# Performance work log

Hardware: AMD Instinct MI355X
Metric: run time of the kernel (lower is better)

Reference implementation:

```python
import jax, jax.numpy as jnp
import numpy as np

B, S, D, H = 4, 2048, 1024, 16
HD = D // H

def setup_inputs() -> dict:
    key = jax.random.key(0)
    ks = jax.random.split(key, 5)
    s = 1.0 / np.sqrt(D)
    return {
        "x": jax.random.normal(ks[0], (B, S, D), dtype=jnp.float32),
        "Wq": jax.random.normal(ks[1], (D, D), dtype=jnp.float32) * s,
        "Wk": jax.random.normal(ks[2], (D, D), dtype=jnp.float32) * s,
        "Wv": jax.random.normal(ks[3], (D, D), dtype=jnp.float32) * s,
        "Wo": jax.random.normal(ks[4], (D, D), dtype=jnp.float32) * s,
        "bo": jnp.zeros((D,), dtype=jnp.float32),
    }

def reference(x, Wq, Wk, Wv, Wo, bo):
    b, n, _ = x.shape
    # torch Linear: x @ W.T ; split heads -> [b, h, n, hd]
    def proj(W):
        return (x @ W.T).reshape(b, n, H, HD).transpose(0, 2, 1, 3)
    q, k, v = proj(Wq), proj(Wk), proj(Wv)
    scores = jnp.einsum('bhqd,bhkd->bhqk', q, k)  # [b,h,n,n]
    causal = jnp.triu(jnp.ones((n, n), dtype=bool), k=1)
    scores = jnp.where(causal, -jnp.inf, scores)
    attn = jax.nn.softmax(scores / np.sqrt(HD), axis=-1)  # dropout p=0.0 (eval)
    ctx = jnp.einsum('bhqk,bhkd->bhqd', attn, v)
    ctx = ctx.transpose(0, 2, 1, 3).reshape(b, n, D)
    return ctx @ Wo.T + bo
```

## Files before the change

### kernel.cpp

```cpp
#include <hip/hip_runtime.h>
#include <stdint.h>
#include <cmath>

#define BATCH 4
#define SEQ   2048
#define DM    1024
#define NH    16
#define HDIM  64
#define MROWS (BATCH*SEQ)

typedef __attribute__((ext_vector_type(8)))  __bf16 bf16x8;
typedef __attribute__((ext_vector_type(8)))  unsigned short u16x8;
typedef __attribute__((ext_vector_type(4)))  float f32x4;
typedef __attribute__((ext_vector_type(16))) float f32x16;
typedef __attribute__((ext_vector_type(4)))  unsigned int u32x4;

__device__ __forceinline__ unsigned short f2bf(float f) {
  unsigned u = __float_as_uint(f);
  u = (u + 0x7FFFu + ((u >> 16) & 1u)) >> 16;
  return (unsigned short)u;
}

__device__ __forceinline__ f32x4 mfma_bf16(bf16x8 a, bf16x8 b, f32x4 c) {
  return __builtin_amdgcn_mfma_f32_16x16x32_bf16(a, b, c, 0, 0, 0);
}
__device__ __forceinline__ f32x16 mfma32(bf16x8 a, bf16x8 b, f32x16 c) {
  return __builtin_amdgcn_mfma_f32_32x32x16_bf16(a, b, c, 0, 0, 0);
}

__device__ __forceinline__ unsigned cvtpk(float lo, float hi) {
  unsigned r;
  asm("v_cvt_pk_bf16_f32 %0, %1, %2" : "=v"(r) : "v"(lo), "v"(hi));
  return r;
}
__device__ __forceinline__ void permswap(unsigned &a, unsigned &b) {
  asm volatile("v_permlane32_swap_b32 %0, %1" : "+v"(a), "+v"(b));
}
__device__ __forceinline__ f32x16 zero16() {
  f32x16 z;
#pragma unroll
  for (int i = 0; i < 16; ++i) z[i] = 0.f;
  return z;
}

typedef const __attribute__((address_space(1))) unsigned int* as1_u32p;
typedef __attribute__((address_space(3))) unsigned int* as3_u32p;

__device__ __forceinline__ void gload16(const void* g, void* l) {
  __builtin_amdgcn_global_load_lds((as1_u32p)g, (as3_u32p)l, 16, 0, 0);
}

__global__ void cvt_f32_bf16(const float* __restrict__ src,
                             unsigned short* __restrict__ dst, int n4) {
  int i = blockIdx.x * blockDim.x + threadIdx.x;
  int stride = gridDim.x * blockDim.x;
  for (; i < n4; i += stride) {
    float4 v = ((const float4*)src)[i];
    ushort4 o;
    o.x = f2bf(v.x); o.y = f2bf(v.y); o.z = f2bf(v.z); o.w = f2bf(v.w);
    ((ushort4*)dst)[i] = o;
  }
}

__device__ __forceinline__ void gemm_tile_mainloop(
    const unsigned short* __restrict__ A, const unsigned short* __restrict__ Bw,
    int rowBase, int colBase,
    unsigned short* As, unsigned short* Bs,
    f32x4 acc[4][4], int tid)
{
  const int wid = tid >> 6, lane = tid & 63;
  const int wm = wid >> 1, wn = wid & 1;
  const unsigned short* Atile = A + (size_t)rowBase * DM;
  const unsigned short* Btile = Bw + (size_t)colBase * DM;

  for (int k0 = 0; k0 < DM; k0 += 64) {
#pragma unroll
    for (int j = 0; j < 4; ++j) {
      int c = j * 256 + tid;
      int row = c >> 3;
      int inB = (c & 7) * 16;
      int srcE = row * DM + k0 + ((inB ^ ((row & 7) << 4)) >> 1);
      gload16(Atile + srcE, As + (size_t)(j * 256 + wid * 64) * 8);
    }
#pragma unroll
    for (int j = 0; j < 4; ++j) {
      int c = j * 256 + tid;
      int row = c >> 3;
      int inB = (c & 7) * 16;
      int srcE = row * DM + k0 + ((inB ^ ((row & 7) << 4)) >> 1);
      gload16(Btile + srcE, Bs + (size_t)(j * 256 + wid * 64) * 8);
    }
    __syncthreads();

#pragma unroll
    for (int s2 = 0; s2 < 2; ++s2) {
      bf16x8 af[4], bfv[4];
#pragma unroll
      for (int m = 0; m < 4; ++m) {
        int row = wm * 64 + m * 16 + (lane & 15);
        int off = row * 128 + ((s2 * 64 + ((lane >> 4) * 16)) ^ ((row & 7) << 4));
        af[m] = *(const bf16x8*)((const char*)As + off);
      }
#pragma unroll
      for (int n = 0; n < 4; ++n) {
        int row = wn * 64 + n * 16 + (lane & 15);
        int off = row * 128 + ((s2 * 64 + ((lane >> 4) * 16)) ^ ((row & 7) << 4));
        bfv[n] = *(const bf16x8*)((const char*)Bs + off);
      }
#pragma unroll
      for (int m = 0; m < 4; ++m)
#pragma unroll
        for (int n = 0; n < 4; ++n)
          acc[m][n] = mfma_bf16(af[m], bfv[n], acc[m][n]);
    }
    __syncthreads();
  }
}

__global__ __launch_bounds__(256, 2) void gemm_qkv(
    const unsigned short* __restrict__ xb,
    const unsigned short* __restrict__ Wqb, const unsigned short* __restrict__ Wkb,
    const unsigned short* __restrict__ Wvb,
    unsigned short* __restrict__ Qd, unsigned short* __restrict__ Kd,
    unsigned short* __restrict__ Vd)
{
  __shared__ unsigned short As[128 * 64];
  __shared__ unsigned short Bs[128 * 64];
  const int tid = threadIdx.x;
  const int z = blockIdx.z;
  const unsigned short* W = (z == 0) ? Wqb : (z == 1) ? Wkb : Wvb;
  unsigned short* dst = (z == 0) ? Qd : (z == 1) ? Kd : Vd;
  const int rowBase = blockIdx.x * 128, colBase = blockIdx.y * 128;

  f32x4 acc[4][4];
#pragma unroll
  for (int m = 0; m < 4; ++m)
#pragma unroll
    for (int n = 0; n < 4; ++n) acc[m][n] = (f32x4){0.f, 0.f, 0.f, 0.f};

  gemm_tile_mainloop(xb, W, rowBase, colBase, As, Bs, acc, tid);

  const int wid = tid >> 6, lane = tid & 63;
  const int wm = wid >> 1, wn = wid & 1;
#pragma unroll
  for (int m = 0; m < 4; ++m)
#pragma unroll
    for (int n = 0; n < 4; ++n)
#pragma unroll
      for (int r = 0; r < 4; ++r) {
        int grow = rowBase + wm * 64 + m * 16 + ((lane >> 4) * 4) + r;
        int gcol = colBase + wn * 64 + n * 16 + (lane & 15);
        int b = grow >> 11, s = grow & (SEQ - 1);
        int h = gcol >> 6, hd = gcol & 63;
        dst[(((size_t)(b * NH + h)) * SEQ + s) * HDIM + hd] = f2bf(acc[m][n][r]);
      }
}

__global__ __launch_bounds__(256, 2) void gemm_out(
    const unsigned short* __restrict__ ctx, const unsigned short* __restrict__ Wob,
    const float* __restrict__ bo, float* __restrict__ out)
{
  __shared__ unsigned short As[128 * 64];
  __shared__ unsigned short Bs[128 * 64];
  const int tid = threadIdx.x;
  const int rowBase = blockIdx.x * 128, colBase = blockIdx.y * 128;

  f32x4 acc[4][4];
#pragma unroll
  for (int m = 0; m < 4; ++m)
#pragma unroll
    for (int n = 0; n < 4; ++n) acc[m][n] = (f32x4){0.f, 0.f, 0.f, 0.f};

  gemm_tile_mainloop(ctx, Wob, rowBase, colBase, As, Bs, acc, tid);

  const int wid = tid >> 6, lane = tid & 63;
  const int wm = wid >> 1, wn = wid & 1;
#pragma unroll
  for (int m = 0; m < 4; ++m)
#pragma unroll
    for (int n = 0; n < 4; ++n)
#pragma unroll
      for (int r = 0; r < 4; ++r) {
        int grow = rowBase + wm * 64 + m * 16 + ((lane >> 4) * 4) + r;
        int gcol = colBase + wn * 64 + n * 16 + (lane & 15);
        out[(size_t)grow * DM + gcol] = acc[m][n][r] + bo[gcol];
      }
}

__global__ void transpose_v(const unsigned short* __restrict__ Vd,
                            unsigned short* __restrict__ VT)
{
  __shared__ unsigned short tile[64 * 72];
  const int tid = threadIdx.x;
  const int bh = blockIdx.y, s0 = blockIdx.x * 64;
  const unsigned short* src = Vd + (size_t)bh * SEQ * HDIM + (size_t)s0 * HDIM;
#pragma unroll
  for (int j = 0; j < 2; ++j) {
    int c = j * 256 + tid;
    int r = c >> 3, c0 = (c & 7) * 8;
    *(u16x8*)(tile + r * 72 + c0) = *(const u16x8*)(src + r * HDIM + c0);
  }
  __syncthreads();
  unsigned short* dst = VT + (size_t)bh * HDIM * SEQ + s0;
#pragma unroll
  for (int j = 0; j < 2; ++j) {
    int c = j * 256 + tid;
    int d = c >> 3, c0 = (c & 7) * 8;
    u16x8 v;
#pragma unroll
    for (int e = 0; e < 8; ++e) v[e] = tile[(c0 + e) * 72 + d];
    *(u16x8*)(dst + (size_t)d * SEQ + c0) = v;
  }
}

__global__ __launch_bounds__(256, 2) void attn_fwd2(
    const unsigned short* __restrict__ Qg, const unsigned short* __restrict__ Kg,
    const unsigned short* __restrict__ VTg, unsigned short* __restrict__ ctx)
{
  __shared__ unsigned short smem[16384];

  const int tid = threadIdx.x, wid = tid >> 6, lane = tid & 63;
  const int hi = lane >> 5, lq = lane & 31;
  const int qb = (int)gridDim.x - 1 - (int)blockIdx.x;
  const int bh = blockIdx.y;
  const unsigned short* Qp = Qg  + (size_t)bh * SEQ * HDIM;
  const unsigned short* Kp = Kg  + (size_t)bh * SEQ * HDIM;
  const unsigned short* Vp = VTg + (size_t)bh * HDIM * SEQ;
  const int qw0 = qb * 128 + wid * 32;

  bf16x8 qf[4];
  {
    const unsigned short* qrow = Qp + (size_t)(qw0 + lq) * HDIM + hi * 8;
#pragma unroll
    for (int ks = 0; ks < 4; ++ks) qf[ks] = *(const bf16x8*)(qrow + ks * 16);
  }

  f32x16 o0 = zero16(), o1 = zero16();
  float m_run = -INFINITY, l_run = 0.f;

  const int nt = 2 * qb + 2;

  auto stageK = [&](int t, int buf) {
#pragma unroll
    for (int j = 0; j < 2; ++j) {
      int c = j * 256 + tid;
      int row = c >> 3, inB = (c & 7) * 16;
      gload16(Kp + (size_t)(t * 64 + row) * HDIM + ((inB ^ ((row & 7) << 4)) >> 1),
              smem + buf * 4096 + (size_t)(j * 256 + wid * 64) * 8);
    }
  };
  auto stageV = [&](int t, int buf) {
#pragma unroll
    for (int j = 0; j < 2; ++j) {
      int c = j * 256 + tid;
      int row = c >> 3, inB = (c & 7) * 16;
      gload16(Vp + (size_t)row * SEQ + t * 64 + ((inB ^ ((row & 7) << 4)) >> 1),
              smem + 8192 + buf * 4096 + (size_t)(j * 256 + wid * 64) * 8);
    }
  };

  stageK(0, 0); stageV(0, 0);
  __syncthreads();

  for (int t = 0; t < nt; ++t) {
    const int cur = t & 1;
    if (t + 1 < nt) { stageK(t + 1, cur ^ 1); stageV(t + 1, cur ^ 1); }

    if (t * 64 <= qw0 + 31) {
      const unsigned short* Kl = smem + cur * 4096;
      f32x16 s0 = zero16(), s1 = zero16();
#pragma unroll
      for (int ks = 0; ks < 4; ++ks) {
        int r0 = lq, r1 = lq + 32;
        int col = (ks * 32 + hi * 16);
        bf16x8 a0 = *(const bf16x8*)((const char*)Kl + r0 * 128 + (col ^ ((r0 & 7) << 4)));
        bf16x8 a1 = *(const bf16x8*)((const char*)Kl + r1 * 128 + (col ^ ((r1 & 7) << 4)));
        s0 = mfma32(a0, qf[ks], s0);
        s1 = mfma32(a1, qf[ks], s1);
      }

      if (t * 64 + 63 > qw0) {
        const int q = qw0 + lq;
        const int kb = t * 64 + 4 * hi;
#pragma unroll
        for (int r = 0; r < 16; ++r) {
          int k0 = kb + (r & 3) + 8 * (r >> 2);
          if (k0 > q)      s0[r] = -INFINITY;
          if (k0 + 32 > q) s1[r] = -INFINITY;
        }
      }

      float pmax = s0[0];
#pragma unroll
      for (int r = 1; r < 16; ++r) pmax = fmaxf(pmax, s0[r]);
#pragma unroll
      for (int r = 0; r < 16; ++r) pmax = fmaxf(pmax, s1[r]);
      pmax = fmaxf(pmax, __shfl_xor(pmax, 32, 64));

      if (!__all(pmax - m_run <= 64.0f)) {
        float mn = fmaxf(m_run, pmax);
        float alpha = __expf((m_run - mn) * 0.125f);
        l_run *= alpha;
#pragma unroll
        for (int r = 0; r < 16; ++r) { o0[r] *= alpha; o1[r] *= alpha; }
        m_run = mn;
      }

      float rsum = 0.f;
#pragma unroll
      for (int r = 0; r < 16; ++r) {
        s0[r] = __expf((s0[r] - m_run) * 0.125f); rsum += s0[r];
      }
#pragma unroll
      for (int r = 0; r < 16; ++r) {
        s1[r] = __expf((s1[r] - m_run) * 0.125f); rsum += s1[r];
      }
      rsum += __shfl_xor(rsum, 32, 64);
      l_run += rsum;

      bf16x8 pfr[4];
#pragma unroll
      for (int h2 = 0; h2 < 2; ++h2) {
        {
          unsigned va = cvtpk(s0[h2 * 8 + 0], s0[h2 * 8 + 1]);
          unsigned vb = cvtpk(s0[h2 * 8 + 4], s0[h2 * 8 + 5]);
          unsigned vc = cvtpk(s0[h2 * 8 + 2], s0[h2 * 8 + 3]);
          unsigned vd = cvtpk(s0[h2 * 8 + 6], s0[h2 * 8 + 7]);
          permswap(va, vb); permswap(vc, vd);
          u32x4 tt; tt.x = va; tt.y = vc; tt.z = vb; tt.w = vd;
          pfr[h2] = __builtin_bit_cast(bf16x8, tt);
        }
        {
          unsigned va = cvtpk(s1[h2 * 8 + 0], s1[h2 * 8 + 1]);
          unsigned vb = cvtpk(s1[h2 * 8 + 4], s1[h2 * 8 + 5]);
          unsigned vc = cvtpk(s1[h2 * 8 + 2], s1[h2 * 8 + 3]);
          unsigned vd = cvtpk(s1[h2 * 8 + 6], s1[h2 * 8 + 7]);
          permswap(va, vb); permswap(vc, vd);
          u32x4 tt; tt.x = va; tt.y = vc; tt.z = vb; tt.w = vd;
          pfr[2 + h2] = __builtin_bit_cast(bf16x8, tt);
        }
      }

      const unsigned short* Vl = smem + 8192 + cur * 4096;
#pragma unroll
      for (int ks = 0; ks < 4; ++ks) {
        int r0 = lq, r1 = lq + 32;
        int col = (ks * 32 + hi * 16);
        bf16x8 va0 = *(const bf16x8*)((const char*)Vl + r0 * 128 + (col ^ ((r0 & 7) << 4)));
        bf16x8 va1 = *(const bf16x8*)((const char*)Vl + r1 * 128 + (col ^ ((r1 & 7) << 4)));
        o0 = mfma32(va0, pfr[ks], o0);
        o1 = mfma32(va1, pfr[ks], o1);
      }
    }
    __syncthreads();
  }

  const float invl = 1.0f / l_run;
  unsigned short* Ot = smem;
  const int q = wid * 32 + lq;
#pragma unroll
  for (int r2 = 0; r2 < 16; r2 += 2) {
    int d = (r2 & 3) + 8 * (r2 >> 2) + 4 * hi;
    unsigned w0 = cvtpk(o0[r2] * invl, o0[r2 + 1] * invl);
    *(unsigned*)((char*)Ot + q * 128 + ((2 * d) ^ ((q & 7) << 4))) = w0;
    int d2 = d + 32;
    unsigned w1 = cvtpk(o1[r2] * invl, o1[r2 + 1] * invl);
    *(unsigned*)((char*)Ot + q * 128 + ((2 * d2) ^ ((q & 7) << 4))) = w1;
  }
  __syncthreads();

  const int b = bh >> 4, h = bh & 15;
#pragma unroll
  for (int i = 0; i < 4; ++i) {
    int idx = i * 256 + tid;
    int qq = idx >> 3, c16 = (idx & 7) * 8;
    bf16x8 v = *(const bf16x8*)((const char*)Ot + qq * 128 + ((2 * c16) ^ ((qq & 7) << 4)));
    *(bf16x8*)(ctx + ((size_t)(b * SEQ) + qb * 128 + qq) * DM + h * 64 + c16) = v;
  }
}

extern "C" void kernel_launch(void* const* d_in, const int* in_sizes, int n_in,
                              void* d_out, int out_size, void* d_ws, size_t ws_size,
                              hipStream_t stream)
{
  (void)in_sizes; (void)n_in; (void)out_size; (void)ws_size;
  const float* x  = (const float*)d_in[0];
  const float* Wq = (const float*)d_in[1];
  const float* Wk = (const float*)d_in[2];
  const float* Wv = (const float*)d_in[3];
  const float* Wo = (const float*)d_in[4];
  const float* bo = (const float*)d_in[5];
  float* out = (float*)d_out;

  char* ws = (char*)d_ws;
  unsigned short* xb  = (unsigned short*)(ws);
  unsigned short* Wqb = (unsigned short*)(ws + (size_t)16 * 1048576);
  unsigned short* Wkb = (unsigned short*)(ws + (size_t)18 * 1048576);
  unsigned short* Wvb = (unsigned short*)(ws + (size_t)20 * 1048576);
  unsigned short* Wob = (unsigned short*)(ws + (size_t)22 * 1048576);
  unsigned short* Qd  = (unsigned short*)(ws + (size_t)24 * 1048576);
  unsigned short* Kd  = (unsigned short*)(ws + (size_t)40 * 1048576);
  unsigned short* Vd  = (unsigned short*)(ws + (size_t)56 * 1048576);
  unsigned short* ctxb= (unsigned short*)(ws + (size_t)72 * 1048576);
  unsigned short* VT  = xb;

  cvt_f32_bf16<<<2048, 256, 0, stream>>>(x,  xb,  MROWS * DM / 4);
  cvt_f32_bf16<<<256,  256, 0, stream>>>(Wq, Wqb, DM * DM / 4);
  cvt_f32_bf16<<<256,  256, 0, stream>>>(Wk, Wkb, DM * DM / 4);
  cvt_f32_bf16<<<256,  256, 0, stream>>>(Wv, Wvb, DM * DM / 4);
  cvt_f32_bf16<<<256,  256, 0, stream>>>(Wo, Wob, DM * DM / 4);

  gemm_qkv<<<dim3(MROWS / 128, DM / 128, 3), 256, 0, stream>>>(xb, Wqb, Wkb, Wvb, Qd, Kd, Vd);
  transpose_v<<<dim3(SEQ / 64, BATCH * NH), 256, 0, stream>>>(Vd, VT);
  attn_fwd2<<<dim3(SEQ / 128, BATCH * NH), 256, 0, stream>>>(Qd, Kd, VT, ctxb);
  gemm_out<<<dim3(MROWS / 128, DM / 128, 1), 256, 0, stream>>>(ctxb, Wob, bo, out);
}
```

Baseline: 291.7 us.

## Pair causal query blocks per CTA, triple-buffer K/V, merge weight conversions

Each attention block now processes two query tiles, qb and NQB-1-qb, so the causal work per CTA is balanced and the grid is halved. K/V staging moves from double to triple buffering, prefetching two tiles ahead with explicit vmcnt waits and raw barriers in place of __syncthreads. MFMA sections are bracketed with s_setprio. The four weight conversion launches are merged into one kernel. The costs are more LDS per block, fewer CTAs (512) for the GPU to spread across its CUs, and the added complexity of hand-written waitcnt accounting.

```diff
diff --git a/kernel.cpp b/kernel.cpp
--- a/kernel.cpp
+++ b/kernel.cpp
@@ -8,6 +8,7 @@
 #define NH    16
 #define HDIM  64
 #define MROWS (BATCH*SEQ)
+#define NQB   16
 
 typedef __attribute__((ext_vector_type(8)))  __bf16 bf16x8;
 typedef __attribute__((ext_vector_type(8)))  unsigned short u16x8;
@@ -62,6 +63,23 @@
   }
 }
 
+__global__ void cvt_w4(const float* __restrict__ s0, const float* __restrict__ s1,
+                       const float* __restrict__ s2, const float* __restrict__ s3,
+                       unsigned short* __restrict__ d0, unsigned short* __restrict__ d1,
+                       unsigned short* __restrict__ d2, unsigned short* __restrict__ d3,
+                       int n4) {
+  const float* src = (blockIdx.y == 0) ? s0 : (blockIdx.y == 1) ? s1 : (blockIdx.y == 2) ? s2 : s3;
+  unsigned short* dst = (blockIdx.y == 0) ? d0 : (blockIdx.y == 1) ? d1 : (blockIdx.y == 2) ? d2 : d3;
+  int i = blockIdx.x * blockDim.x + threadIdx.x;
+  int stride = gridDim.x * blockDim.x;
+  for (; i < n4; i += stride) {
+    float4 v = ((const float4*)src)[i];
+    ushort4 o;
+    o.x = f2bf(v.x); o.y = f2bf(v.y); o.z = f2bf(v.z); o.w = f2bf(v.w);
+    ((ushort4*)dst)[i] = o;
+  }
+}
+
 __device__ __forceinline__ void gemm_tile_mainloop(
     const unsigned short* __restrict__ A, const unsigned short* __restrict__ Bw,
     int rowBase, int colBase,
@@ -213,32 +231,19 @@
   }
 }
 
-__global__ __launch_bounds__(256, 2) void attn_fwd2(
+__global__ __launch_bounds__(256, 2) void attn_fwd3(
     const unsigned short* __restrict__ Qg, const unsigned short* __restrict__ Kg,
     const unsigned short* __restrict__ VTg, unsigned short* __restrict__ ctx)
 {
-  __shared__ unsigned short smem[16384];
+  __shared__ unsigned short smem[24576];
 
   const int tid = threadIdx.x, wid = tid >> 6, lane = tid & 63;
   const int hi = lane >> 5, lq = lane & 31;
-  const int qb = (int)gridDim.x - 1 - (int)blockIdx.x;
   const int bh = blockIdx.y;
   const unsigned short* Qp = Qg  + (size_t)bh * SEQ * HDIM;
   const unsigned short* Kp = Kg  + (size_t)bh * SEQ * HDIM;
   const unsigned short* Vp = VTg + (size_t)bh * HDIM * SEQ;
-  const int qw0 = qb * 128 + wid * 32;
-
-  bf16x8 qf[4];
-  {
-    const unsigned short* qrow = Qp + (size_t)(qw0 + lq) * HDIM + hi * 8;
-#pragma unroll
-    for (int ks = 0; ks < 4; ++ks) qf[ks] = *(const bf16x8*)(qrow + ks * 16);
-  }
-
-  f32x16 o0 = zero16(), o1 = zero16();
-  float m_run = -INFINITY, l_run = 0.f;
-
-  const int nt = 2 * qb + 2;
+  const int b = bh >> 4, h = bh & 15;
 
   auto stageK = [&](int t, int buf) {
 #pragma unroll
@@ -255,127 +260,153 @@
       int c = j * 256 + tid;
       int row = c >> 3, inB = (c & 7) * 16;
       gload16(Vp + (size_t)row * SEQ + t * 64 + ((inB ^ ((row & 7) << 4)) >> 1),
-              smem + 8192 + buf * 4096 + (size_t)(j * 256 + wid * 64) * 8);
+              smem + 12288 + buf * 4096 + (size_t)(j * 256 + wid * 64) * 8);
     }
   };
 
-  stageK(0, 0); stageV(0, 0);
-  __syncthreads();
-
-  for (int t = 0; t < nt; ++t) {
-    const int cur = t & 1;
-    if (t + 1 < nt) { stageK(t + 1, cur ^ 1); stageV(t + 1, cur ^ 1); }
-
-    if (t * 64 <= qw0 + 31) {
-      const unsigned short* Kl = smem + cur * 4096;
-      f32x16 s0 = zero16(), s1 = zero16();
-#pragma unroll
-      for (int ks = 0; ks < 4; ++ks) {
-        int r0 = lq, r1 = lq + 32;
-        int col = (ks * 32 + hi * 16);
-        bf16x8 a0 = *(const bf16x8*)((const char*)Kl + r0 * 128 + (col ^ ((r0 & 7) << 4)));
-        bf16x8 a1 = *(const bf16x8*)((const char*)Kl + r1 * 128 + (col ^ ((r1 & 7) << 4)));
-        s0 = mfma32(a0, qf[ks], s0);
-        s1 = mfma32(a1, qf[ks], s1);
+  for (int half = 0; half < 2; ++half) {
+    const int qb = half == 0 ? (int)blockIdx.x : (NQB - 1 - (int)blockIdx.x);
+    const int qw0 = qb * 128 + wid * 32;
+
+    bf16x8 qf[4];
+    {
+      const unsigned short* qrow = Qp + (size_t)(qw0 + lq) * HDIM + hi * 8;
+#pragma unroll
+      for (int ks = 0; ks < 4; ++ks) qf[ks] = *(const bf16x8*)(qrow + ks * 16);
+    }
+
+    f32x16 o0 = zero16(), o1 = zero16();
+    float m_run = -INFINITY, l_run = 0.f;
+    const int nt = 2 * qb + 2;
+
+    stageK(0, 0); stageV(0, 0);
+    stageK(1, 1); stageV(1, 1);
+    asm volatile("s_waitcnt vmcnt(4)" ::: "memory");
+    __builtin_amdgcn_s_barrier();
+
+    for (int t = 0; t < nt; ++t) {
+      const int cur = t % 3;
+      const bool pf = (t + 2) < nt;
+      if (pf) { int nb = (t + 2) % 3; stageK(t + 2, nb); stageV(t + 2, nb); }
+
+      if (t * 64 <= qw0 + 31) {
+        const unsigned short* Kl = smem + cur * 4096;
+        f32x16 s0 = zero16(), s1 = zero16();
+        __builtin_amdgcn_s_setprio(1);
+#pragma unroll
+        for (int ks = 0; ks < 4; ++ks) {
+          int r0 = lq, r1 = lq + 32;
+          int col = (ks * 32 + hi * 16);
+          bf16x8 a0 = *(const bf16x8*)((const char*)Kl + r0 * 128 + (col ^ ((r0 & 7) << 4)));
+          bf16x8 a1 = *(const bf16x8*)((const char*)Kl + r1 * 128 + (col ^ ((r1 & 7) << 4)));
+          s0 = mfma32(a0, qf[ks], s0);
+          s1 = mfma32(a1, qf[ks], s1);
+        }
+        __builtin_amdgcn_s_setprio(0);
+
+        if (t * 64 + 63 > qw0) {
+          const int q = qw0 + lq;
+          const int kb = t * 64 + 4 * hi;
+#pragma unroll
+          for (int r = 0; r < 16; ++r) {
+            int k0 = kb + (r & 3) + 8 * (r >> 2);
+            if (k0 > q)      s0[r] = -INFINITY;
+            if (k0 + 32 > q) s1[r] = -INFINITY;
+          }
+        }
+
+        float pmax = s0[0];
+#pragma unroll
+        for (int r = 1; r < 16; ++r) pmax = fmaxf(pmax, s0[r]);
+#pragma unroll
+        for (int r = 0; r < 16; ++r) pmax = fmaxf(pmax, s1[r]);
+        pmax = fmaxf(pmax, __shfl_xor(pmax, 32, 64));
+
+        if (!__all(pmax - m_run <= 64.0f)) {
+          float mn = fmaxf(m_run, pmax);
+          float alpha = __expf((m_run - mn) * 0.125f);
+          l_run *= alpha;
+#pragma unroll
+          for (int r = 0; r < 16; ++r) { o0[r] *= alpha; o1[r] *= alpha; }
+          m_run = mn;
+        }
+
+        float rsum = 0.f;
+#pragma unroll
+        for (int r = 0; r < 16; ++r) {
+          s0[r] = __expf((s0[r] - m_run) * 0.125f); rsum += s0[r];
+        }
+#pragma unroll
+        for (int r = 0; r < 16; ++r) {
+          s1[r] = __expf((s1[r] - m_run) * 0.125f); rsum += s1[r];
+        }
+        rsum += __shfl_xor(rsum, 32, 64);
+        l_run += rsum;
+
+        bf16x8 pfr[4];
+#pragma unroll
+        for (int h2 = 0; h2 < 2; ++h2) {
+          {
+            unsigned va = cvtpk(s0[h2 * 8 + 0], s0[h2 * 8 + 1]);
+            unsigned vb = cvtpk(s0[h2 * 8 + 4], s0[h2 * 8 + 5]);
+            unsigned vc = cvtpk(s0[h2 * 8 + 2], s0[h2 * 8 + 3]);
+            unsigned vd = cvtpk(s0[h2 * 8 + 6], s0[h2 * 8 + 7]);
+            permswap(va, vb); permswap(vc, vd);
+            u32x4 tt; tt.x = va; tt.y = vc; tt.z = vb; tt.w = vd;
+            pfr[h2] = __builtin_bit_cast(bf16x8, tt);
+          }
+          {
+            unsigned va = cvtpk(s1[h2 * 8 + 0], s1[h2 * 8 + 1]);
+            unsigned vb = cvtpk(s1[h2 * 8 + 4], s1[h2 * 8 + 5]);
+            unsigned vc = cvtpk(s1[h2 * 8 + 2], s1[h2 * 8 + 3]);
+            unsigned vd = cvtpk(s1[h2 * 8 + 6], s1[h2 * 8 + 7]);
+            permswap(va, vb); permswap(vc, vd);
+            u32x4 tt; tt.x = va; tt.y = vc; tt.z = vb; tt.w = vd;
+            pfr[2 + h2] = __builtin_bit_cast(bf16x8, tt);
+          }
+        }
+
+        const unsigned short* Vl = smem + 12288 + cur * 4096;
+        __builtin_amdgcn_s_setprio(1);
+#pragma unroll
+        for (int ks = 0; ks < 4; ++ks) {
+          int r0 = lq, r1 = lq + 32;
+          int col = (ks * 32 + hi * 16);
+          bf16x8 va0 = *(const bf16x8*)((const char*)Vl + r0 * 128 + (col ^ ((r0 & 7) << 4)));
+          bf16x8 va1 = *(const bf16x8*)((const char*)Vl + r1 * 128 + (col ^ ((r1 & 7) << 4)));
+          o0 = mfma32(va0, pfr[ks], o0);
+          o1 = mfma32(va1, pfr[ks], o1);
+        }
+        __builtin_amdgcn_s_setprio(0);
       }
 
-      if (t * 64 + 63 > qw0) {
-        const int q = qw0 + lq;
-        const int kb = t * 64 + 4 * hi;
-#pragma unroll
-        for (int r = 0; r < 16; ++r) {
-          int k0 = kb + (r & 3) + 8 * (r >> 2);
-          if (k0 > q)      s0[r] = -INFINITY;
-          if (k0 + 32 > q) s1[r] = -INFINITY;
-        }
-      }
-
-      float pmax = s0[0];
-#pragma unroll
-      for (int r = 1; r < 16; ++r) pmax = fmaxf(pmax, s0[r]);
-#pragma unroll
-      for (int r = 0; r < 16; ++r) pmax = fmaxf(pmax, s1[r]);
-      pmax = fmaxf(pmax, __shfl_xor(pmax, 32, 64));
-
-      if (!__all(pmax - m_run <= 64.0f)) {
-        float mn = fmaxf(m_run, pmax);
-        float alpha = __expf((m_run - mn) * 0.125f);
-        l_run *= alpha;
-#pragma unroll
-        for (int r = 0; r < 16; ++r) { o0[r] *= alpha; o1[r] *= alpha; }
-        m_run = mn;
-      }
-
-      float rsum = 0.f;
-#pragma unroll
-      for (int r = 0; r < 16; ++r) {
-        s0[r] = __expf((s0[r] - m_run) * 0.125f); rsum += s0[r];
-      }
-#pragma unroll
-      for (int r = 0; r < 16; ++r) {
-        s1[r] = __expf((s1[r] - m_run) * 0.125f); rsum += s1[r];
-      }
-      rsum += __shfl_xor(rsum, 32, 64);
-      l_run += rsum;
-
-      bf16x8 pfr[4];
-#pragma unroll
-      for (int h2 = 0; h2 < 2; ++h2) {
-        {
-          unsigned va = cvtpk(s0[h2 * 8 + 0], s0[h2 * 8 + 1]);
-          unsigned vb = cvtpk(s0[h2 * 8 + 4], s0[h2 * 8 + 5]);
-          unsigned vc = cvtpk(s0[h2 * 8 + 2], s0[h2 * 8 + 3]);
-          unsigned vd = cvtpk(s0[h2 * 8 + 6], s0[h2 * 8 + 7]);
-          permswap(va, vb); permswap(vc, vd);
-          u32x4 tt; tt.x = va; tt.y = vc; tt.z = vb; tt.w = vd;
-          pfr[h2] = __builtin_bit_cast(bf16x8, tt);
-        }
-        {
-          unsigned va = cvtpk(s1[h2 * 8 + 0], s1[h2 * 8 + 1]);
-          unsigned vb = cvtpk(s1[h2 * 8 + 4], s1[h2 * 8 + 5]);
-          unsigned vc = cvtpk(s1[h2 * 8 + 2], s1[h2 * 8 + 3]);
-          unsigned vd = cvtpk(s1[h2 * 8 + 6], s1[h2 * 8 + 7]);
-          permswap(va, vb); permswap(vc, vd);
-          u32x4 tt; tt.x = va; tt.y = vc; tt.z = vb; tt.w = vd;
-          pfr[2 + h2] = __builtin_bit_cast(bf16x8, tt);
-        }
-      }
-
-      const unsigned short* Vl = smem + 8192 + cur * 4096;
-#pragma unroll
-      for (int ks = 0; ks < 4; ++ks) {
-        int r0 = lq, r1 = lq + 32;
-        int col = (ks * 32 + hi * 16);
-        bf16x8 va0 = *(const bf16x8*)((const char*)Vl + r0 * 128 + (col ^ ((r0 & 7) << 4)));
-        bf16x8 va1 = *(const bf16x8*)((const char*)Vl + r1 * 128 + (col ^ ((r1 & 7) << 4)));
-        o0 = mfma32(va0, pfr[ks], o0);
-        o1 = mfma32(va1, pfr[ks], o1);
-      }
+      if (pf) asm volatile("s_waitcnt vmcnt(4)" ::: "memory");
+      else    asm volatile("s_waitcnt vmcnt(0)" ::: "memory");
+      __builtin_amdgcn_s_barrier();
+    }
+
+    const float invl = 1.0f / l_run;
+    unsigned short* Ot = smem;
+    const int q = wid * 32 + lq;
+#pragma unroll
+    for (int r2 = 0; r2 < 16; r2 += 2) {
+      int d = (r2 & 3) + 8 * (r2 >> 2) + 4 * hi;
+      unsigned w0 = cvtpk(o0[r2] * invl, o0[r2 + 1] * invl);
+      *(unsigned*)((char*)Ot + q * 128 + ((2 * d) ^ ((q & 7) << 4))) = w0;
+      int d2 = d + 32;
+      unsigned w1 = cvtpk(o1[r2] * invl, o1[r2 + 1] * invl);
+      *(unsigned*)((char*)Ot + q * 128 + ((2 * d2) ^ ((q & 7) << 4))) = w1;
     }
     __syncthreads();
-  }
-
-  const float invl = 1.0f / l_run;
-  unsigned short* Ot = smem;
-  const int q = wid * 32 + lq;
-#pragma unroll
-  for (int r2 = 0; r2 < 16; r2 += 2) {
-    int d = (r2 & 3) + 8 * (r2 >> 2) + 4 * hi;
-    unsigned w0 = cvtpk(o0[r2] * invl, o0[r2 + 1] * invl);
-    *(unsigned*)((char*)Ot + q * 128 + ((2 * d) ^ ((q & 7) << 4))) = w0;
-    int d2 = d + 32;
-    unsigned w1 = cvtpk(o1[r2] * invl, o1[r2 + 1] * invl);
-    *(unsigned*)((char*)Ot + q * 128 + ((2 * d2) ^ ((q & 7) << 4))) = w1;
-  }
-  __syncthreads();
-
-  const int b = bh >> 4, h = bh & 15;
-#pragma unroll
-  for (int i = 0; i < 4; ++i) {
-    int idx = i * 256 + tid;
-    int qq = idx >> 3, c16 = (idx & 7) * 8;
-    bf16x8 v = *(const bf16x8*)((const char*)Ot + qq * 128 + ((2 * c16) ^ ((qq & 7) << 4)));
-    *(bf16x8*)(ctx + ((size_t)(b * SEQ) + qb * 128 + qq) * DM + h * 64 + c16) = v;
+
+#pragma unroll
+    for (int i = 0; i < 4; ++i) {
+      int idx = i * 256 + tid;
+      int qq = idx >> 3, c16 = (idx & 7) * 8;
+      bf16x8 v = *(const bf16x8*)((const char*)Ot + qq * 128 + ((2 * c16) ^ ((qq & 7) << 4)));
+      *(bf16x8*)(ctx + ((size_t)(b * SEQ) + qb * 128 + qq) * DM + h * 64 + c16) = v;
+    }
+    __syncthreads();
   }
 }
 
@@ -404,14 +435,11 @@
   unsigned short* ctxb= (unsigned short*)(ws + (size_t)72 * 1048576);
   unsigned short* VT  = xb;
 
-  cvt_f32_bf16<<<2048, 256, 0, stream>>>(x,  xb,  MROWS * DM / 4);
-  cvt_f32_bf16<<<256,  256, 0, stream>>>(Wq, Wqb, DM * DM / 4);
-  cvt_f32_bf16<<<256,  256, 0, stream>>>(Wk, Wkb, DM * DM / 4);
-  cvt_f32_bf16<<<256,  256, 0, stream>>>(Wv, Wvb, DM * DM / 4);
-  cvt_f32_bf16<<<256,  256, 0, stream>>>(Wo, Wob, DM * DM / 4);
+  cvt_f32_bf16<<<2048, 256, 0, stream>>>(x, xb, MROWS * DM / 4);
+  cvt_w4<<<dim3(64, 4), 256, 0, stream>>>(Wq, Wk, Wv, Wo, Wqb, Wkb, Wvb, Wob, DM * DM / 4);
 
   gemm_qkv<<<dim3(MROWS / 128, DM / 128, 3), 256, 0, stream>>>(xb, Wqb, Wkb, Wvb, Qd, Kd, Vd);
   transpose_v<<<dim3(SEQ / 64, BATCH * NH), 256, 0, stream>>>(Vd, VT);
-  attn_fwd2<<<dim3(SEQ / 128, BATCH * NH), 256, 0, stream>>>(Qd, Kd, VT, ctxb);
+  attn_fwd3<<<dim3(NQB / 2, BATCH * NH), 256, 0, stream>>>(Qd, Kd, VT, ctxb);
   gemm_out<<<dim3(MROWS / 128, DM / 128, 1), 256, 0, stream>>>(ctxb, Wob, bo, out);
 }
```

New measurement: 242.3 us. -16.9%, faster.
